# Kernel tuning notes

Hardware: AMD Instinct MI355X
Metric: run time of the kernel (lower is better)

## Reference

```python
import jax, jax.numpy as jnp
import numpy as np

N = 100000   # nodes
E = 100000   # hyperedges
M = 1600000  # incidences
IN_C = 128
HID = 128
OUT_C = 64
L = 2
EPS = 1e-5


def _layer_norm(x, g, b):
    m = jnp.mean(x, axis=-1, keepdims=True)
    v = jnp.mean((x - m) ** 2, axis=-1, keepdims=True)
    return (x - m) * jax.lax.rsqrt(v + EPS) * g + b


def setup_inputs() -> dict:
    key = jax.random.key(0)
    ks = jax.random.split(key, 16)
    s_in = 1.0 / np.sqrt(IN_C)
    s_h = 1.0 / np.sqrt(HID)
    return {
        "x": jax.random.normal(ks[0], (N, IN_C), jnp.float32),
        "x_e": jax.random.normal(ks[1], (E, IN_C), jnp.float32),
        "edge_index": jax.random.randint(ks[2], (2, M), 0, N, jnp.int32),
        "in_norm_g": jnp.ones((IN_C,), jnp.float32),
        "in_norm_b": jnp.zeros((IN_C,), jnp.float32),
        "in_proj_W": jax.random.normal(ks[3], (IN_C, HID), jnp.float32) * s_in,
        "in_proj_b": jnp.zeros((HID,), jnp.float32),
        "norm_g": jnp.ones((L, HID), jnp.float32),
        "norm_b": jnp.zeros((L, HID), jnp.float32),
        "conv_W": jax.random.normal(ks[4], (L, HID, HID), jnp.float32) * s_h,
        "conv_b": jnp.zeros((L, HID), jnp.float32),
        "lin_W": jax.random.normal(ks[5], (HID, OUT_C), jnp.float32) * s_h,
        "lin_b": jnp.zeros((OUT_C,), jnp.float32),
    }


def reference(x, x_e, edge_index, in_norm_g, in_norm_b, in_proj_W, in_proj_b,
              norm_g, norm_b, conv_W, conv_b, lin_W, lin_b):
    src, dst = edge_index[0], edge_index[1]  # node ids, hyperedge ids
    h = _layer_norm(x, in_norm_g, in_norm_b)
    h = jax.nn.leaky_relu(h @ in_proj_W + in_proj_b)  # dropout = identity (eval)

    # HypergraphConv degree normalizers (hyperedge_weight = 1)
    ones = jnp.ones((M,), h.dtype)
    degD = jax.ops.segment_sum(ones, src, num_segments=N)
    D = jnp.where(degD > 0, 1.0 / degD, 0.0)          # [N]
    degB = jax.ops.segment_sum(ones, dst, num_segments=E)
    B = jnp.where(degB > 0, 1.0 / degB, 0.0)          # [E]

    for i in range(L):
        hn = _layer_norm(h, norm_g[i], norm_b[i])
        xw = hn @ conv_W[i]                            # [N, HID]
        # node -> hyperedge: sum_j B[e] * xw[j]
        he = jax.ops.segment_sum(B[dst][:, None] * xw[src], dst, num_segments=E)
        # hyperedge -> node: sum_e D[n] * he[e]
        h2 = jax.ops.segment_sum(D[src][:, None] * he[dst], src, num_segments=N)
        h = jax.nn.leaky_relu(h2 + conv_b[i])

    # MinAggregation: segment-min of gathered node features per hyperedge
    agg = jax.ops.segment_min(h[src], dst, num_segments=E)  # [E, HID]
    return agg @ lin_W + lin_b                              # [E, OUT_C]
```

## Files before the change

kernel.cpp:

```cpp
#include <hip/hip_runtime.h>

#define NN 100000
#define NE 100000
#define MI 1600000
#define HID 128
#define OUTC 64
#define LSLOPE 0.01f
#define EPSV 1e-5f
#define ADJ_STRIDE 48
#define BUILD_PASSES 10
#define BUILD_WIN ((NN + BUILD_PASSES - 1) / BUILD_PASSES)

typedef __attribute__((ext_vector_type(4))) unsigned short us4;
typedef __attribute__((ext_vector_type(8))) short short8;
typedef __attribute__((ext_vector_type(16))) float f32x16;

__device__ __forceinline__ float bf2f(unsigned short h) {
    return __uint_as_float(((unsigned)h) << 16);
}
__device__ __forceinline__ unsigned short f2bf(float f) {
    unsigned u = __float_as_uint(f);
    return (unsigned short)((u + 0x7FFFu + ((u >> 16) & 1u)) >> 16);
}

__global__ void build_win_kernel(const int* __restrict__ ei,
                                 int* __restrict__ cntE, int* __restrict__ cntN,
                                 int* __restrict__ adjE, int* __restrict__ adjN,
                                 int lo, int hi) {
    int m = blockIdx.x * blockDim.x + threadIdx.x;
    if (m >= MI) return;
    int s = ei[m], d = ei[MI + m];
    if (d >= lo && d < hi) {
        int p = atomicAdd(&cntE[d], 1);
        if (p < ADJ_STRIDE) adjE[d * ADJ_STRIDE + p] = s;
    }
    if (s >= lo && s < hi) {
        int p = atomicAdd(&cntN[s], 1);
        if (p < ADJ_STRIDE) adjN[s * ADJ_STRIDE + p] = d;
    }
}

__global__ void recip_kernel(const int* __restrict__ deg, float* __restrict__ out, int n) {
    int i = blockIdx.x * blockDim.x + threadIdx.x;
    if (i < n) { int d = deg[i]; out[i] = d > 0 ? 1.0f / (float)d : 0.0f; }
}

__global__ void tconv_kernel(const float* __restrict__ src, unsigned short* __restrict__ hi,
                             unsigned short* __restrict__ lo, int K, int N) {
    int idx = blockIdx.x * blockDim.x + threadIdx.x;
    if (idx >= K * N) return;
    int n = idx / K, k = idx - n * K;
    float v = src[k * N + n];
    unsigned short h = f2bf(v);
    hi[idx] = h;
    if (lo) lo[idx] = f2bf(v - bf2f(h));
}

template <int MODE>
__global__ __launch_bounds__(256) void gather_kernel(
    const int* __restrict__ cnt, const int* __restrict__ adj,
    const unsigned short* __restrict__ src, const float* __restrict__ scale,
    const float* __restrict__ bias, unsigned short* __restrict__ dst, int R)
{
    int g = threadIdx.x >> 5;
    int lane = threadIdx.x & 31;
    int r = blockIdx.x * 8 + g;
    if (r >= R) return;
    int n = cnt[r]; n = n < ADJ_STRIDE ? n : ADJ_STRIDE;
    const int* arow = adj + (size_t)r * ADJ_STRIDE;
    float ax, ay, az, aw;
    if (MODE == 2) { ax = ay = az = aw = INFINITY; }
    else           { ax = ay = az = aw = 0.f; }
    const unsigned short* base = src + lane * 4;
    int j = 0;
    for (; j + 3 < n; j += 4) {
        int i0 = arow[j], i1 = arow[j + 1], i2 = arow[j + 2], i3 = arow[j + 3];
        us4 v0 = *(const us4*)(base + (size_t)i0 * HID);
        us4 v1 = *(const us4*)(base + (size_t)i1 * HID);
        us4 v2 = *(const us4*)(base + (size_t)i2 * HID);
        us4 v3 = *(const us4*)(base + (size_t)i3 * HID);
        if (MODE == 2) {
            ax = fminf(ax, fminf(fminf(bf2f(v0.x), bf2f(v1.x)), fminf(bf2f(v2.x), bf2f(v3.x))));
            ay = fminf(ay, fminf(fminf(bf2f(v0.y), bf2f(v1.y)), fminf(bf2f(v2.y), bf2f(v3.y))));
            az = fminf(az, fminf(fminf(bf2f(v0.z), bf2f(v1.z)), fminf(bf2f(v2.z), bf2f(v3.z))));
            aw = fminf(aw, fminf(fminf(bf2f(v0.w), bf2f(v1.w)), fminf(bf2f(v2.w), bf2f(v3.w))));
        } else {
            ax += (bf2f(v0.x) + bf2f(v1.x)) + (bf2f(v2.x) + bf2f(v3.x));
            ay += (bf2f(v0.y) + bf2f(v1.y)) + (bf2f(v2.y) + bf2f(v3.y));
            az += (bf2f(v0.z) + bf2f(v1.z)) + (bf2f(v2.z) + bf2f(v3.z));
            aw += (bf2f(v0.w) + bf2f(v1.w)) + (bf2f(v2.w) + bf2f(v3.w));
        }
    }
    for (; j < n; ++j) {
        int i0 = arow[j];
        us4 v0 = *(const us4*)(base + (size_t)i0 * HID);
        if (MODE == 2) {
            ax = fminf(ax, bf2f(v0.x)); ay = fminf(ay, bf2f(v0.y));
            az = fminf(az, bf2f(v0.z)); aw = fminf(aw, bf2f(v0.w));
        } else {
            ax += bf2f(v0.x); ay += bf2f(v0.y); az += bf2f(v0.z); aw += bf2f(v0.w);
        }
    }
    if (MODE == 0) {
        float s = scale[r];
        ax *= s; ay *= s; az *= s; aw *= s;
    } else if (MODE == 1) {
        float s = scale[r];
        float4 b = *(const float4*)(bias + lane * 4);
        float x;
        x = s * ax + b.x; ax = x > 0.f ? x : LSLOPE * x;
        x = s * ay + b.y; ay = x > 0.f ? x : LSLOPE * x;
        x = s * az + b.z; az = x > 0.f ? x : LSLOPE * x;
        x = s * aw + b.w; aw = x > 0.f ? x : LSLOPE * x;
    }
    us4 o;
    o.x = f2bf(ax); o.y = f2bf(ay); o.z = f2bf(az); o.w = f2bf(aw);
    *(us4*)(dst + (size_t)r * HID + lane * 4) = o;
}

template <int NC, bool ABF16, bool OBF16, bool SPLIT>
__global__ __launch_bounds__(512) void mfma_gemm_kernel(
    const void* __restrict__ Av, const float* __restrict__ ln_g, const float* __restrict__ ln_b,
    const unsigned short* __restrict__ WT, const float* __restrict__ bias,
    void* __restrict__ outv, int R, int flags)
{
    constexpr int SA = 136;
    constexpr int NW = (SPLIT ? 2 : 1) * NC;
    constexpr int CT = NC / 64;
    __shared__ unsigned short As[128 * SA];
    __shared__ unsigned short Ws[NW * SA];
    __shared__ float red_s[512];
    __shared__ float red_q[512];
    __shared__ float r_mean[128];
    __shared__ float r_rstd[128];

    const int t = threadIdx.x;
    const int row0 = blockIdx.x * 128;

    constexpr int WUS4 = NW * 128 / 4;
    #pragma unroll
    for (int i = t; i < WUS4; i += 512) {
        us4 w = ((const us4*)WT)[i];
        int nrow = i >> 5, k4 = i & 31;
        *(us4*)(Ws + nrow * SA + k4 * 4) = w;
    }

    {
        const int r = t >> 2, sub = t & 3;
        const int gr = row0 + r;
        float v[32];
        if (gr < R) {
            if (ABF16) {
                const unsigned short* ap = (const unsigned short*)Av + (size_t)gr * 128 + sub * 32;
                #pragma unroll
                for (int j4 = 0; j4 < 8; ++j4) {
                    us4 x4 = *(const us4*)(ap + j4 * 4);
                    v[j4 * 4 + 0] = bf2f(x4.x); v[j4 * 4 + 1] = bf2f(x4.y);
                    v[j4 * 4 + 2] = bf2f(x4.z); v[j4 * 4 + 3] = bf2f(x4.w);
                }
            } else {
                const float* ap = (const float*)Av + (size_t)gr * 128 + sub * 32;
                #pragma unroll
                for (int j4 = 0; j4 < 8; ++j4) {
                    float4 f4 = *(const float4*)(ap + j4 * 4);
                    v[j4 * 4 + 0] = f4.x; v[j4 * 4 + 1] = f4.y;
                    v[j4 * 4 + 2] = f4.z; v[j4 * 4 + 3] = f4.w;
                }
            }
        } else {
            #pragma unroll
            for (int j = 0; j < 32; ++j) v[j] = 0.f;
        }
        if (flags & 1) {
            float s = 0.f, q = 0.f;
            #pragma unroll
            for (int j = 0; j < 32; ++j) { s += v[j]; q += v[j] * v[j]; }
            red_s[t] = s; red_q[t] = q;
            __syncthreads();
            if (t < 128) {
                float ss = red_s[t * 4] + red_s[t * 4 + 1] + red_s[t * 4 + 2] + red_s[t * 4 + 3];
                float qq = red_q[t * 4] + red_q[t * 4 + 1] + red_q[t * 4 + 2] + red_q[t * 4 + 3];
                float mu = ss * (1.0f / 128.0f);
                float var = qq * (1.0f / 128.0f) - mu * mu;
                r_mean[t] = mu;
                r_rstd[t] = rsqrtf(var + EPSV);
            }
            __syncthreads();
            float mu = r_mean[r], rs = r_rstd[r];
            #pragma unroll
            for (int j4 = 0; j4 < 8; ++j4) {
                float4 g4 = *(const float4*)(ln_g + sub * 32 + j4 * 4);
                float4 b4 = *(const float4*)(ln_b + sub * 32 + j4 * 4);
                v[j4 * 4 + 0] = (v[j4 * 4 + 0] - mu) * rs * g4.x + b4.x;
                v[j4 * 4 + 1] = (v[j4 * 4 + 1] - mu) * rs * g4.y + b4.y;
                v[j4 * 4 + 2] = (v[j4 * 4 + 2] - mu) * rs * g4.z + b4.z;
                v[j4 * 4 + 3] = (v[j4 * 4 + 3] - mu) * rs * g4.w + b4.w;
            }
        }
        #pragma unroll
        for (int j4 = 0; j4 < 8; ++j4) {
            us4 o;
            o.x = f2bf(v[j4 * 4 + 0]); o.y = f2bf(v[j4 * 4 + 1]);
            o.z = f2bf(v[j4 * 4 + 2]); o.w = f2bf(v[j4 * 4 + 3]);
            *(us4*)(As + r * SA + sub * 32 + j4 * 4) = o;
        }
    }
    __syncthreads();

    const int lane = t & 63;
    const int wave = t >> 6;
    const int wr = (wave & 3) * 32;
    const int wc = (wave >> 2) * (NC / 2);
    const int m = lane & 31;
    const int half = lane >> 5;
    const unsigned short* a_base = As + (wr + m) * SA + half * 8;

    f32x16 acc[CT];
    #pragma unroll
    for (int ct = 0; ct < CT; ++ct) acc[ct] = (f32x16)(0.0f);

    #pragma unroll
    for (int ks = 0; ks < 8; ++ks) {
        short8 a = *(const short8*)(a_base + ks * 16);
        #pragma unroll
        for (int ct = 0; ct < CT; ++ct) {
            const unsigned short* b_base = Ws + (wc + ct * 32 + m) * SA + half * 8 + ks * 16;
            short8 b = *(const short8*)b_base;
            acc[ct] = __builtin_amdgcn_mfma_f32_32x32x16_bf16(a, b, acc[ct], 0, 0, 0);
            if (SPLIT) {
                short8 bl = *(const short8*)(b_base + (size_t)NC * SA);
                acc[ct] = __builtin_amdgcn_mfma_f32_32x32x16_bf16(a, bl, acc[ct], 0, 0, 0);
            }
        }
    }

    #pragma unroll
    for (int ct = 0; ct < CT; ++ct) {
        int gc = wc + ct * 32 + m;
        float bv = bias ? bias[gc] : 0.f;
        #pragma unroll
        for (int reg = 0; reg < 16; ++reg) {
            int rloc = (reg & 3) + 8 * (reg >> 2) + 4 * half;
            int gr = row0 + wr + rloc;
            if (gr < R) {
                float y = acc[ct][reg] + bv;
                if (flags & 4) y = y > 0.f ? y : LSLOPE * y;
                if (OBF16) ((unsigned short*)outv)[(size_t)gr * NC + gc] = f2bf(y);
                else       ((float*)outv)[(size_t)gr * NC + gc] = y;
            }
        }
    }
}

extern "C" void kernel_launch(void* const* d_in, const int* in_sizes, int n_in,
                              void* d_out, int out_size, void* d_ws, size_t ws_size,
                              hipStream_t stream) {
    const float* x      = (const float*)d_in[0];
    const int*   ei     = (const int*)d_in[2];
    const float* in_g   = (const float*)d_in[3];
    const float* in_b   = (const float*)d_in[4];
    const float* in_W   = (const float*)d_in[5];
    const float* in_pb  = (const float*)d_in[6];
    const float* norm_g = (const float*)d_in[7];
    const float* norm_b = (const float*)d_in[8];
    const float* conv_W = (const float*)d_in[9];
    const float* conv_b = (const float*)d_in[10];
    const float* lin_W  = (const float*)d_in[11];
    const float* lin_b  = (const float*)d_in[12];
    float* out = (float*)d_out;

    unsigned short* h_bf   = (unsigned short*)d_ws;
    unsigned short* xw_bf  = h_bf  + (size_t)NN * HID;
    unsigned short* he_bf  = xw_bf + (size_t)NN * HID;
    unsigned short* agg_bf = he_bf + (size_t)NE * HID;
    float* D    = (float*)(agg_bf + (size_t)NE * HID);
    float* B    = D + NN;
    int* cntE   = (int*)(B + NE);
    int* cntN   = cntE + NE;
    int* adjE   = cntN + NN;
    int* adjN   = adjE + (size_t)NE * ADJ_STRIDE;
    unsigned short* wt_in  = (unsigned short*)(adjN + (size_t)NN * ADJ_STRIDE);
    unsigned short* wt_c0  = wt_in + 128 * 128;
    unsigned short* wt_c1  = wt_c0 + 128 * 128;
    unsigned short* wt_lin = wt_c1 + 128 * 128;

    hipMemsetAsync(cntE, 0, (size_t)(NN + NE) * sizeof(int), stream);
    for (int p = 0; p < BUILD_PASSES; ++p) {
        int lo = p * BUILD_WIN;
        int hi = lo + BUILD_WIN < NN ? lo + BUILD_WIN : NN;
        build_win_kernel<<<(MI + 255) / 256, 256, 0, stream>>>(ei, cntE, cntN, adjE, adjN, lo, hi);
    }
    recip_kernel<<<(NN + 255) / 256, 256, 0, stream>>>(cntN, D, NN);
    recip_kernel<<<(NE + 255) / 256, 256, 0, stream>>>(cntE, B, NE);

    tconv_kernel<<<(128 * 128 + 255) / 256, 256, 0, stream>>>(in_W, wt_in, nullptr, 128, 128);
    tconv_kernel<<<(128 * 128 + 255) / 256, 256, 0, stream>>>(conv_W, wt_c0, nullptr, 128, 128);
    tconv_kernel<<<(128 * 128 + 255) / 256, 256, 0, stream>>>(conv_W + 128 * 128, wt_c1, nullptr, 128, 128);
    tconv_kernel<<<(128 * 64 + 255) / 256, 256, 0, stream>>>(lin_W, wt_lin, wt_lin + 64 * 128, 128, 64);

    mfma_gemm_kernel<HID, false, true, false><<<(NN + 127) / 128, 512, 0, stream>>>(
        x, in_g, in_b, wt_in, in_pb, h_bf, NN, 1 | 4);

    for (int i = 0; i < 2; ++i) {
        mfma_gemm_kernel<HID, true, true, false><<<(NN + 127) / 128, 512, 0, stream>>>(
            h_bf, norm_g + i * HID, norm_b + i * HID, i ? wt_c1 : wt_c0,
            nullptr, xw_bf, NN, 1);
        gather_kernel<0><<<(NE + 7) / 8, 256, 0, stream>>>(cntE, adjE, xw_bf, B, nullptr, he_bf, NE);
        gather_kernel<1><<<(NN + 7) / 8, 256, 0, stream>>>(cntN, adjN, he_bf, D, conv_b + i * HID, h_bf, NN);
    }

    gather_kernel<2><<<(NE + 7) / 8, 256, 0, stream>>>(cntE, adjE, h_bf, nullptr, nullptr, agg_bf, NE);

    mfma_gemm_kernel<OUTC, true, false, true><<<(NE + 127) / 128, 512, 0, stream>>>(
        agg_bf, nullptr, nullptr, wt_lin, lin_b, out, NE, 0);
}
```

Before: 809.1 us.

## Fuse prep kernels, cut build passes, and unroll gather loop by eight

```diff
diff --git a/kernel.cpp b/kernel.cpp
--- a/kernel.cpp
+++ b/kernel.cpp
@@ -8,19 +8,20 @@
 #define LSLOPE 0.01f
 #define EPSV 1e-5f
 #define ADJ_STRIDE 48
-#define BUILD_PASSES 10
+#define BUILD_PASSES 6
 #define BUILD_WIN ((NN + BUILD_PASSES - 1) / BUILD_PASSES)
 
+typedef unsigned short us;
 typedef __attribute__((ext_vector_type(4))) unsigned short us4;
 typedef __attribute__((ext_vector_type(8))) short short8;
 typedef __attribute__((ext_vector_type(16))) float f32x16;
 
-__device__ __forceinline__ float bf2f(unsigned short h) {
+__device__ __forceinline__ float bf2f(us h) {
     return __uint_as_float(((unsigned)h) << 16);
 }
-__device__ __forceinline__ unsigned short f2bf(float f) {
+__device__ __forceinline__ us f2bf(float f) {
     unsigned u = __float_as_uint(f);
-    return (unsigned short)((u + 0x7FFFu + ((u >> 16) & 1u)) >> 16);
+    return (us)((u + 0x7FFFu + ((u >> 16) & 1u)) >> 16);
 }
 
 __global__ void build_win_kernel(const int* __restrict__ ei,
@@ -40,27 +41,43 @@
     }
 }
 
-__global__ void recip_kernel(const int* __restrict__ deg, float* __restrict__ out, int n) {
+__global__ void recip2_kernel(const int* __restrict__ cntE, const int* __restrict__ cntN,
+                              float* __restrict__ B, float* __restrict__ D) {
     int i = blockIdx.x * blockDim.x + threadIdx.x;
-    if (i < n) { int d = deg[i]; out[i] = d > 0 ? 1.0f / (float)d : 0.0f; }
-}
-
-__global__ void tconv_kernel(const float* __restrict__ src, unsigned short* __restrict__ hi,
-                             unsigned short* __restrict__ lo, int K, int N) {
+    if (i < NE) {
+        int d = cntE[i]; B[i] = d > 0 ? 1.0f / (float)d : 0.0f;
+    } else if (i < NE + NN) {
+        int j = i - NE;
+        int d = cntN[j]; D[j] = d > 0 ? 1.0f / (float)d : 0.0f;
+    }
+}
+
+__global__ void wprep_kernel(const float* __restrict__ in_W, const float* __restrict__ conv_W,
+                             const float* __restrict__ lin_W,
+                             us* __restrict__ wt_in, us* __restrict__ wt_c0,
+                             us* __restrict__ wt_c1, us* __restrict__ wt_lin) {
     int idx = blockIdx.x * blockDim.x + threadIdx.x;
-    if (idx >= K * N) return;
-    int n = idx / K, k = idx - n * K;
-    float v = src[k * N + n];
-    unsigned short h = f2bf(v);
-    hi[idx] = h;
-    if (lo) lo[idx] = f2bf(v - bf2f(h));
+    if (idx < 49152) {
+        int mat = idx >> 14, r = idx & 16383;
+        const float* src = mat == 0 ? in_W : (mat == 1 ? conv_W : conv_W + 16384);
+        us* dst = mat == 0 ? wt_in : (mat == 1 ? wt_c0 : wt_c1);
+        int n = r >> 7, k = r & 127;
+        dst[r] = f2bf(src[k * 128 + n]);
+    } else if (idx < 57344) {
+        int r = idx - 49152;
+        int n = r >> 7, k = r & 127;
+        float v = lin_W[k * 64 + n];
+        us h = f2bf(v);
+        wt_lin[r] = h;
+        wt_lin[8192 + r] = f2bf(v - bf2f(h));
+    }
 }
 
 template <int MODE>
 __global__ __launch_bounds__(256) void gather_kernel(
     const int* __restrict__ cnt, const int* __restrict__ adj,
-    const unsigned short* __restrict__ src, const float* __restrict__ scale,
-    const float* __restrict__ bias, unsigned short* __restrict__ dst, int R)
+    const us* __restrict__ src, const float* __restrict__ scale,
+    const float* __restrict__ bias, us* __restrict__ dst, int R)
 {
     int g = threadIdx.x >> 5;
     int lane = threadIdx.x & 31;
@@ -71,29 +88,54 @@
     float ax, ay, az, aw;
     if (MODE == 2) { ax = ay = az = aw = INFINITY; }
     else           { ax = ay = az = aw = 0.f; }
-    const unsigned short* base = src + lane * 4;
+    const us* base = src + lane * 4;
     int j = 0;
-    for (; j + 3 < n; j += 4) {
-        int i0 = arow[j], i1 = arow[j + 1], i2 = arow[j + 2], i3 = arow[j + 3];
-        us4 v0 = *(const us4*)(base + (size_t)i0 * HID);
-        us4 v1 = *(const us4*)(base + (size_t)i1 * HID);
-        us4 v2 = *(const us4*)(base + (size_t)i2 * HID);
-        us4 v3 = *(const us4*)(base + (size_t)i3 * HID);
+    for (; j + 7 < n; j += 8) {
+        us4 v0 = *(const us4*)(base + (size_t)arow[j]     * HID);
+        us4 v1 = *(const us4*)(base + (size_t)arow[j + 1] * HID);
+        us4 v2 = *(const us4*)(base + (size_t)arow[j + 2] * HID);
+        us4 v3 = *(const us4*)(base + (size_t)arow[j + 3] * HID);
+        us4 v4 = *(const us4*)(base + (size_t)arow[j + 4] * HID);
+        us4 v5 = *(const us4*)(base + (size_t)arow[j + 5] * HID);
+        us4 v6 = *(const us4*)(base + (size_t)arow[j + 6] * HID);
+        us4 v7 = *(const us4*)(base + (size_t)arow[j + 7] * HID);
         if (MODE == 2) {
-            ax = fminf(ax, fminf(fminf(bf2f(v0.x), bf2f(v1.x)), fminf(bf2f(v2.x), bf2f(v3.x))));
-            ay = fminf(ay, fminf(fminf(bf2f(v0.y), bf2f(v1.y)), fminf(bf2f(v2.y), bf2f(v3.y))));
-            az = fminf(az, fminf(fminf(bf2f(v0.z), bf2f(v1.z)), fminf(bf2f(v2.z), bf2f(v3.z))));
-            aw = fminf(aw, fminf(fminf(bf2f(v0.w), bf2f(v1.w)), fminf(bf2f(v2.w), bf2f(v3.w))));
+            ax = fminf(ax, fminf(fminf(fminf(bf2f(v0.x), bf2f(v1.x)), fminf(bf2f(v2.x), bf2f(v3.x))),
+                                 fminf(fminf(bf2f(v4.x), bf2f(v5.x)), fminf(bf2f(v6.x), bf2f(v7.x)))));
+            ay = fminf(ay, fminf(fminf(fminf(bf2f(v0.y), bf2f(v1.y)), fminf(bf2f(v2.y), bf2f(v3.y))),
+                                 fminf(fminf(bf2f(v4.y), bf2f(v5.y)), fminf(bf2f(v6.y), bf2f(v7.y)))));
+            az = fminf(az, fminf(fminf(fminf(bf2f(v0.z), bf2f(v1.z)), fminf(bf2f(v2.z), bf2f(v3.z))),
+                                 fminf(fminf(bf2f(v4.z), bf2f(v5.z)), fminf(bf2f(v6.z), bf2f(v7.z)))));
+            aw = fminf(aw, fminf(fminf(fminf(bf2f(v0.w), bf2f(v1.w)), fminf(bf2f(v2.w), bf2f(v3.w))),
+                                 fminf(fminf(bf2f(v4.w), bf2f(v5.w)), fminf(bf2f(v6.w), bf2f(v7.w)))));
         } else {
-            ax += (bf2f(v0.x) + bf2f(v1.x)) + (bf2f(v2.x) + bf2f(v3.x));
-            ay += (bf2f(v0.y) + bf2f(v1.y)) + (bf2f(v2.y) + bf2f(v3.y));
-            az += (bf2f(v0.z) + bf2f(v1.z)) + (bf2f(v2.z) + bf2f(v3.z));
-            aw += (bf2f(v0.w) + bf2f(v1.w)) + (bf2f(v2.w) + bf2f(v3.w));
-        }
-    }
-    for (; j < n; ++j) {
-        int i0 = arow[j];
-        us4 v0 = *(const us4*)(base + (size_t)i0 * HID);
+            ax += ((bf2f(v0.x) + bf2f(v1.x)) + (bf2f(v2.x) + bf2f(v3.x)))
+                + ((bf2f(v4.x) + bf2f(v5.x)) + (bf2f(v6.x) + bf2f(v7.x)));
+            ay += ((bf2f(v0.y) + bf2f(v1.y)) + (bf2f(v2.y) + bf2f(v3.y)))
+                + ((bf2f(v4.y) + bf2f(v5.y)) + (bf2f(v6.y) + bf2f(v7.y)));
+            az += ((bf2f(v0.z) + bf2f(v1.z)) + (bf2f(v2.z) + bf2f(v3.z)))
+                + ((bf2f(v4.z) + bf2f(v5.z)) + (bf2f(v6.z) + bf2f(v7.z)));
+            aw += ((bf2f(v0.w) + bf2f(v1.w)) + (bf2f(v2.w) + bf2f(v3.w)))
+                + ((bf2f(v4.w) + bf2f(v5.w)) + (bf2f(v6.w) + bf2f(v7.w)));
+        }
+    }
+    for (; j + 1 < n; j += 2) {
+        us4 v0 = *(const us4*)(base + (size_t)arow[j]     * HID);
+        us4 v1 = *(const us4*)(base + (size_t)arow[j + 1] * HID);
+        if (MODE == 2) {
+            ax = fminf(ax, fminf(bf2f(v0.x), bf2f(v1.x)));
+            ay = fminf(ay, fminf(bf2f(v0.y), bf2f(v1.y)));
+            az = fminf(az, fminf(bf2f(v0.z), bf2f(v1.z)));
+            aw = fminf(aw, fminf(bf2f(v0.w), bf2f(v1.w)));
+        } else {
+            ax += bf2f(v0.x) + bf2f(v1.x);
+            ay += bf2f(v0.y) + bf2f(v1.y);
+            az += bf2f(v0.z) + bf2f(v1.z);
+            aw += bf2f(v0.w) + bf2f(v1.w);
+        }
+    }
+    if (j < n) {
+        us4 v0 = *(const us4*)(base + (size_t)arow[j] * HID);
         if (MODE == 2) {
             ax = fminf(ax, bf2f(v0.x)); ay = fminf(ay, bf2f(v0.y));
             az = fminf(az, bf2f(v0.z)); aw = fminf(aw, bf2f(v0.w));
@@ -121,14 +163,14 @@
 template <int NC, bool ABF16, bool OBF16, bool SPLIT>
 __global__ __launch_bounds__(512) void mfma_gemm_kernel(
     const void* __restrict__ Av, const float* __restrict__ ln_g, const float* __restrict__ ln_b,
-    const unsigned short* __restrict__ WT, const float* __restrict__ bias,
+    const us* __restrict__ WT, const float* __restrict__ bias,
     void* __restrict__ outv, int R, int flags)
 {
     constexpr int SA = 136;
     constexpr int NW = (SPLIT ? 2 : 1) * NC;
     constexpr int CT = NC / 64;
-    __shared__ unsigned short As[128 * SA];
-    __shared__ unsigned short Ws[NW * SA];
+    __shared__ us As[128 * SA];
+    __shared__ us Ws[NW * SA];
     __shared__ float red_s[512];
     __shared__ float red_q[512];
     __shared__ float r_mean[128];
@@ -151,7 +193,7 @@
         float v[32];
         if (gr < R) {
             if (ABF16) {
-                const unsigned short* ap = (const unsigned short*)Av + (size_t)gr * 128 + sub * 32;
+                const us* ap = (const us*)Av + (size_t)gr * 128 + sub * 32;
                 #pragma unroll
                 for (int j4 = 0; j4 < 8; ++j4) {
                     us4 x4 = *(const us4*)(ap + j4 * 4);
@@ -213,7 +255,7 @@
     const int wc = (wave >> 2) * (NC / 2);
     const int m = lane & 31;
     const int half = lane >> 5;
-    const unsigned short* a_base = As + (wr + m) * SA + half * 8;
+    const us* a_base = As + (wr + m) * SA + half * 8;
 
     f32x16 acc[CT];
     #pragma unroll
@@ -224,7 +266,7 @@
         short8 a = *(const short8*)(a_base + ks * 16);
         #pragma unroll
         for (int ct = 0; ct < CT; ++ct) {
-            const unsigned short* b_base = Ws + (wc + ct * 32 + m) * SA + half * 8 + ks * 16;
+            const us* b_base = Ws + (wc + ct * 32 + m) * SA + half * 8 + ks * 16;
             short8 b = *(const short8*)b_base;
             acc[ct] = __builtin_amdgcn_mfma_f32_32x32x16_bf16(a, b, acc[ct], 0, 0, 0);
             if (SPLIT) {
@@ -245,7 +287,7 @@
             if (gr < R) {
                 float y = acc[ct][reg] + bv;
                 if (flags & 4) y = y > 0.f ? y : LSLOPE * y;
-                if (OBF16) ((unsigned short*)outv)[(size_t)gr * NC + gc] = f2bf(y);
+                if (OBF16) ((us*)outv)[(size_t)gr * NC + gc] = f2bf(y);
                 else       ((float*)outv)[(size_t)gr * NC + gc] = y;
             }
         }
@@ -269,20 +311,20 @@
     const float* lin_b  = (const float*)d_in[12];
     float* out = (float*)d_out;
 
-    unsigned short* h_bf   = (unsigned short*)d_ws;
-    unsigned short* xw_bf  = h_bf  + (size_t)NN * HID;
-    unsigned short* he_bf  = xw_bf + (size_t)NN * HID;
-    unsigned short* agg_bf = he_bf + (size_t)NE * HID;
+    us* h_bf   = (us*)d_ws;
+    us* xw_bf  = h_bf  + (size_t)NN * HID;
+    us* he_bf  = xw_bf + (size_t)NN * HID;
+    us* agg_bf = he_bf + (size_t)NE * HID;
     float* D    = (float*)(agg_bf + (size_t)NE * HID);
     float* B    = D + NN;
     int* cntE   = (int*)(B + NE);
     int* cntN   = cntE + NE;
     int* adjE   = cntN + NN;
     int* adjN   = adjE + (size_t)NE * ADJ_STRIDE;
-    unsigned short* wt_in  = (unsigned short*)(adjN + (size_t)NN * ADJ_STRIDE);
-    unsigned short* wt_c0  = wt_in + 128 * 128;
-    unsigned short* wt_c1  = wt_c0 + 128 * 128;
-    unsigned short* wt_lin = wt_c1 + 128 * 128;
+    us* wt_in  = (us*)(adjN + (size_t)NN * ADJ_STRIDE);
+    us* wt_c0  = wt_in + 128 * 128;
+    us* wt_c1  = wt_c0 + 128 * 128;
+    us* wt_lin = wt_c1 + 128 * 128;
 
     hipMemsetAsync(cntE, 0, (size_t)(NN + NE) * sizeof(int), stream);
     for (int p = 0; p < BUILD_PASSES; ++p) {
@@ -290,13 +332,10 @@
         int hi = lo + BUILD_WIN < NN ? lo + BUILD_WIN : NN;
         build_win_kernel<<<(MI + 255) / 256, 256, 0, stream>>>(ei, cntE, cntN, adjE, adjN, lo, hi);
     }
-    recip_kernel<<<(NN + 255) / 256, 256, 0, stream>>>(cntN, D, NN);
-    recip_kernel<<<(NE + 255) / 256, 256, 0, stream>>>(cntE, B, NE);
-
-    tconv_kernel<<<(128 * 128 + 255) / 256, 256, 0, stream>>>(in_W, wt_in, nullptr, 128, 128);
-    tconv_kernel<<<(128 * 128 + 255) / 256, 256, 0, stream>>>(conv_W, wt_c0, nullptr, 128, 128);
-    tconv_kernel<<<(128 * 128 + 255) / 256, 256, 0, stream>>>(conv_W + 128 * 128, wt_c1, nullptr, 128, 128);
-    tconv_kernel<<<(128 * 64 + 255) / 256, 256, 0, stream>>>(lin_W, wt_lin, wt_lin + 64 * 128, 128, 64);
+    recip2_kernel<<<(NN + NE + 255) / 256, 256, 0, stream>>>(cntE, cntN, B, D);
+
+    wprep_kernel<<<(57344 + 255) / 256, 256, 0, stream>>>(
+        in_W, conv_W, lin_W, wt_in, wt_c0, wt_c1, wt_lin);
 
     mfma_gemm_kernel<HID, false, true, false><<<(NN + 127) / 128, 512, 0, stream>>>(
         x, in_g, in_b, wt_in, in_pb, h_bf, NN, 1 | 4);
```

After: 757.8 us. -6.3%, faster.
